# Optimization experiments

Measured on AMD Instinct MI355X. Metric: run time of the kernel, lower is better.

## Reference

```python
import jax, jax.numpy as jnp
import numpy as np

H, KV, HD, HID = 32, 8, 128, 4096
THETA, FACTOR, HI_FF, LO_FF, ORIG_MAX = 500000.0, 8.0, 4.0, 1.0, 8192


def _llama3_inv_freq():
    # standard Llama-3 rope scaling
    inv = 1.0 / (THETA ** (np.arange(0, HD, 2, dtype=np.float64) / HD))
    wavelen = 2.0 * np.pi / inv
    low_wl = ORIG_MAX / LO_FF
    high_wl = ORIG_MAX / HI_FF
    smooth = (ORIG_MAX / wavelen - LO_FF) / (HI_FF - LO_FF)
    scaled = np.where(wavelen > low_wl, inv / FACTOR, inv)
    mid = (wavelen <= low_wl) & (wavelen >= high_wl)
    scaled = np.where(mid, (1 - smooth) * inv / FACTOR + smooth * inv, scaled)
    return scaled.astype(np.float32)


def _rope_cos_sin(T):
    inv = _llama3_inv_freq()                       # [HD/2]
    pos = np.arange(T, dtype=np.float32)
    freqs = pos[:, None] * inv[None, :]            # [T, HD/2]
    emb = np.concatenate([freqs, freqs], axis=-1)  # [T, HD]
    return jnp.asarray(np.cos(emb)), jnp.asarray(np.sin(emb))


def _rotate_half(x):
    x1, x2 = jnp.split(x, 2, axis=-1)
    return jnp.concatenate([-x2, x1], axis=-1)


def setup_inputs() -> dict:
    key = jax.random.key(0)
    ks = jax.random.split(key, 5)
    s = 1.0 / np.sqrt(HID)
    return {
        "x": jax.random.normal(ks[0], (1, 2048, HID), jnp.float32),
        "wq": jax.random.normal(ks[1], (HID, H * HD), jnp.float32) * s,
        "wk": jax.random.normal(ks[2], (HID, KV * HD), jnp.float32) * s,
        "wv": jax.random.normal(ks[3], (HID, KV * HD), jnp.float32) * s,
        "wo": jax.random.normal(ks[4], (H * HD, HID), jnp.float32) * s,
    }


def reference(x, wq, wk, wv, wo):
    B, T, _ = x.shape
    q = (x @ wq).reshape(B, T, H, HD).transpose(0, 2, 1, 3)   # [B,H,T,D]
    k = (x @ wk).reshape(B, T, KV, HD).transpose(0, 2, 1, 3)  # [B,KV,T,D]
    v = (x @ wv).reshape(B, T, KV, HD).transpose(0, 2, 1, 3)
    cos, sin = _rope_cos_sin(T)                               # [T,D]
    q = q * cos + _rotate_half(q) * sin
    k = k * cos + _rotate_half(k) * sin
    rep = H // KV
    k = jnp.repeat(k, rep, axis=1)                            # [B,H,T,D]
    v = jnp.repeat(v, rep, axis=1)
    scores = jnp.einsum("bhtd,bhsd->bhts", q, k) * (1.0 / np.sqrt(HD))
    mask = jnp.tril(jnp.ones((T, T), dtype=bool))
    scores = jnp.where(mask, scores, -jnp.inf)
    att = jax.nn.softmax(scores, axis=-1)
    out = jnp.einsum("bhts,bhsd->bhtd", att, v)
    out = out.transpose(0, 2, 1, 3).reshape(B, T, H * HD)
    return out @ wo
```

## Files before the change

kernel.cpp:

```cpp
#include <hip/hip_runtime.h>
#include <math.h>

#define T_SEQ 2048
#define HID   4096
#define NH    32
#define NKV   8
#define HD    128
#define QCOLS (NH*HD)
#define KCOLS (NKV*HD)
#define KSTR  2048

typedef _Float16 f16;
typedef _Float16 f16x8 __attribute__((ext_vector_type(8)));
typedef _Float16 f16x4 __attribute__((ext_vector_type(4)));
typedef float f32x4 __attribute__((ext_vector_type(4)));

#define GLDS(g, l) __builtin_amdgcn_global_load_lds( \
    (const __attribute__((address_space(1))) void*)(g), \
    (__attribute__((address_space(3))) void*)(l), 16, 0, 0)

__global__ void rope_table(float* __restrict__ cosT, float* __restrict__ sinT) {
    int idx = blockIdx.x * blockDim.x + threadIdx.x;
    if (idx >= T_SEQ * 64) return;
    int t = idx >> 6, i = idx & 63;
    double inv = pow(500000.0, -(double)(2 * i) / 128.0);
    double wavelen = 6.283185307179586 / inv;
    const double lowwl = 8192.0, highwl = 2048.0;
    double scaled;
    if (wavelen > lowwl) {
        scaled = inv / 8.0;
    } else if (wavelen >= highwl) {
        double smooth = (8192.0 / wavelen - 1.0) / 3.0;
        scaled = (1.0 - smooth) * inv / 8.0 + smooth * inv;
    } else {
        scaled = inv;
    }
    float invf = (float)scaled;
    float phase = (float)t * invf;
    cosT[idx] = (float)cos((double)phase);
    sinT[idx] = (float)sin((double)phase);
}

__global__ void convert_f32_f16(const float* __restrict__ in, f16* __restrict__ out, int n8) {
    int i = blockIdx.x * blockDim.x + threadIdx.x;
    if (i >= n8) return;
    float4 a = *(const float4*)(in + (size_t)i * 8);
    float4 b = *(const float4*)(in + (size_t)i * 8 + 4);
    f16x8 v = {(f16)a.x, (f16)a.y, (f16)a.z, (f16)a.w, (f16)b.x, (f16)b.y, (f16)b.z, (f16)b.w};
    *(f16x8*)(out + (size_t)i * 8) = v;
}

__global__ __launch_bounds__(256) void transpose_f32_to_f16(const float* __restrict__ in,
                                                            f16* __restrict__ out,
                                                            int R, int ld) {
    __shared__ f16 t[64][72];
    const int tid = threadIdx.x;
    const int r0 = blockIdx.y * 64, c0 = blockIdx.x * 64;
#pragma unroll
    for (int i = 0; i < 4; ++i) {
        int r = i * 16 + (tid >> 4), c4 = (tid & 15) * 4;
        float4 v = *(const float4*)(in + (size_t)(r0 + r) * ld + c0 + c4);
        t[r][c4 + 0] = (f16)v.x; t[r][c4 + 1] = (f16)v.y;
        t[r][c4 + 2] = (f16)v.z; t[r][c4 + 3] = (f16)v.w;
    }
    __syncthreads();
    int n = tid >> 2, j0 = (tid & 3) * 16;
    f16x8 a, b;
#pragma unroll
    for (int j = 0; j < 8; ++j) { a[j] = t[j0 + j][n]; b[j] = t[j0 + 8 + j][n]; }
    *(f16x8*)(out + (size_t)(c0 + n) * R + r0 + j0) = a;
    *(f16x8*)(out + (size_t)(c0 + n) * R + r0 + j0 + 8) = b;
}

__global__ __launch_bounds__(256) void transpose_f16(const f16* __restrict__ in,
                                                     f16* __restrict__ out,
                                                     int R, int ld) {
    __shared__ f16 t[64][72];
    const int tid = threadIdx.x;
    const int r0 = blockIdx.y * 64, c0 = blockIdx.x * 64;
#pragma unroll
    for (int i = 0; i < 2; ++i) {
        int r = i * 32 + (tid >> 3), c8 = (tid & 7) * 8;
        f16x8 v = *(const f16x8*)(in + (size_t)(r0 + r) * ld + c0 + c8);
#pragma unroll
        for (int j = 0; j < 8; ++j) t[r][c8 + j] = v[j];
    }
    __syncthreads();
    int n = tid >> 2, j0 = (tid & 3) * 16;
    f16x8 a, b;
#pragma unroll
    for (int j = 0; j < 8; ++j) { a[j] = t[j0 + j][n]; b[j] = t[j0 + 8 + j][n]; }
    *(f16x8*)(out + (size_t)(c0 + n) * R + r0 + j0) = a;
    *(f16x8*)(out + (size_t)(c0 + n) * R + r0 + j0 + 8) = b;
}

template <typename OutT>
__global__ __launch_bounds__(256, 2) void gemm_f16(const f16* __restrict__ A,
                                                   const f16* __restrict__ Bt,
                                                   OutT* __restrict__ C,
                                                   int M, int ldc, int K) {
    __shared__ f16 As[2][128 * 64];
    __shared__ f16 Bs[2][128 * 64];
    const int tid = threadIdx.x;
    const int l = tid & 63;
    const int w = tid >> 6, wr = w >> 1, wc = w & 1;
    const int c16 = l & 15, g = l >> 4;
    const int m0 = blockIdx.y * 128, n0 = blockIdx.x * 128;

    f32x4 acc[4][4] = {};

    const int r_src = tid >> 3;
    const int colswz = ((tid & 7) * 8) ^ ((r_src & 7) << 3);
    const f16* gA = A + (size_t)(m0 + r_src) * K + colswz;
    const f16* gB = Bt + (size_t)(n0 + r_src) * K + colswz;

    auto stage = [&](f16* sA, f16* sB, int k0) {
#pragma unroll
        for (int i = 0; i < 4; ++i) {
            GLDS(gA + (size_t)(i * 32) * K + k0, sA + i * 2048 + tid * 8);
            GLDS(gB + (size_t)(i * 32) * K + k0, sB + i * 2048 + tid * 8);
        }
    };
    auto compute = [&](const f16* sA, const f16* sB) {
#pragma unroll
        for (int kk = 0; kk < 2; ++kk) {
            f16x8 af[4], bf[4];
#pragma unroll
            for (int mb = 0; mb < 4; ++mb) {
                int row = wr * 64 + mb * 16 + c16;
                af[mb] = *(const f16x8*)((const char*)sA + row * 128 +
                                         ((kk * 64 + g * 16) ^ ((row & 7) << 4)));
            }
#pragma unroll
            for (int nb = 0; nb < 4; ++nb) {
                int row = wc * 64 + nb * 16 + c16;
                bf[nb] = *(const f16x8*)((const char*)sB + row * 128 +
                                         ((kk * 64 + g * 16) ^ ((row & 7) << 4)));
            }
#pragma unroll
            for (int mb = 0; mb < 4; ++mb)
#pragma unroll
                for (int nb = 0; nb < 4; ++nb)
                    acc[mb][nb] = __builtin_amdgcn_mfma_f32_16x16x32_f16(af[mb], bf[nb], acc[mb][nb], 0, 0, 0);
        }
    };

    stage(As[0], Bs[0], 0);
    __syncthreads();
    int cur = 0;
    for (int k0 = 64; k0 < K; k0 += 64) {
        stage(As[cur ^ 1], Bs[cur ^ 1], k0);
        compute(As[cur], Bs[cur]);
        __syncthreads();
        cur ^= 1;
    }
    compute(As[cur], Bs[cur]);

#pragma unroll
    for (int mb = 0; mb < 4; ++mb)
#pragma unroll
        for (int nb = 0; nb < 4; ++nb)
#pragma unroll
            for (int r = 0; r < 4; ++r) {
                size_t row = m0 + wr * 64 + mb * 16 + g * 4 + r;
                C[row * ldc + n0 + wc * 64 + nb * 16 + c16] = (OutT)acc[mb][nb][r];
            }
}

__global__ void rope_apply_f16(f16* __restrict__ data, const float* __restrict__ cosT,
                               const float* __restrict__ sinT, int nheads, int stride) {
    int idx = blockIdx.x * blockDim.x + threadIdx.x;
    int lane = idx & 63;
    int row = idx >> 6;
    if (row >= T_SEQ * nheads) return;
    int t = row / nheads, h = row % nheads;
    f16* p = data + (size_t)t * stride + h * HD;
    float c = cosT[t * 64 + lane], s = sinT[t * 64 + lane];
    float x1 = (float)p[lane], x2 = (float)p[lane + 64];
    p[lane]      = (f16)(x1 * c - x2 * s);
    p[lane + 64] = (f16)(x2 * c + x1 * s);
}

__global__ __launch_bounds__(256, 2) void attn_f16(const f16* __restrict__ q,
                                                   const f16* __restrict__ k,
                                                   const f16* __restrict__ vt,
                                                   const float* __restrict__ cosT,
                                                   const float* __restrict__ sinT,
                                                   f16* __restrict__ outh) {
    __shared__ f16 Ks[2][64 * 128];
    __shared__ f16 Vs[2][128 * 64];
    __shared__ f16 Ps[4][16 * 72];
    const int tid = threadIdx.x;
    const int l = tid & 63, w = tid >> 6;
    const int c16 = l & 15, g = l >> 4;
    const int h = blockIdx.y, kvh = h >> 2;
    const float SCALE = 0.08838834764831845f;

    const int kr = tid >> 4, kboff = (tid & 15) * 16;
    const int vr = tid >> 3, vboff = (tid & 7) * 16;
    const char* kgb = (const char*)(k + kvh * HD);
    const char* vgb = (const char*)(vt + (size_t)(kvh * HD) * T_SEQ);

    auto stage = [&](int buf, int ch) {
#pragma unroll
        for (int i = 0; i < 4; ++i) {
            int r = i * 16 + kr;
            GLDS(kgb + (size_t)(ch * 64 + r) * (KSTR * 2) + (kboff ^ ((r & 7) << 4)),
                 (char*)Ks[buf] + i * 4096 + tid * 16);
            int d = i * 32 + vr;
            GLDS(vgb + (size_t)d * (T_SEQ * 2) + (size_t)(ch * 64) * 2 + (vboff ^ ((d & 7) << 4)),
                 (char*)Vs[buf] + i * 4096 + tid * 16);
        }
    };

    for (int pass = 0; pass < 2; ++pass) {
        const int qt = pass ? 31 - (int)blockIdx.x : (int)blockIdx.x;
        const int qrow = qt * 64 + w * 16 + c16;

        f16x8 qf[4];
        {
            const f16* qbase = q + (size_t)qrow * QCOLS + h * HD;
            f16x8 qraw[4];
#pragma unroll
            for (int ks = 0; ks < 4; ++ks) qraw[ks] = *(const f16x8*)(qbase + ks * 32 + g * 8);
            const float* cb = cosT + qrow * 64;
            const float* sb = sinT + qrow * 64;
#pragma unroll
            for (int ks = 0; ks < 2; ++ks) {
                int dbase = ks * 32 + g * 8;
                float4 c0 = *(const float4*)(cb + dbase);
                float4 c1 = *(const float4*)(cb + dbase + 4);
                float4 s0 = *(const float4*)(sb + dbase);
                float4 s1 = *(const float4*)(sb + dbase + 4);
                float cA[8] = {c0.x, c0.y, c0.z, c0.w, c1.x, c1.y, c1.z, c1.w};
                float sA[8] = {s0.x, s0.y, s0.z, s0.w, s1.x, s1.y, s1.z, s1.w};
#pragma unroll
                for (int j = 0; j < 8; ++j) {
                    float lo = (float)qraw[ks][j], hi = (float)qraw[ks + 2][j];
                    qf[ks][j]     = (f16)(lo * cA[j] - hi * sA[j]);
                    qf[ks + 2][j] = (f16)(hi * cA[j] + lo * sA[j]);
                }
            }
        }

        f32x4 o[8] = {};
        float mrun = -INFINITY, lrun = 0.f;

        stage(0, 0);
        __syncthreads();
        int cur = 0;
        for (int ch = 0; ch <= qt; ++ch) {
            if (ch < qt) stage(cur ^ 1, ch + 1);

            f32x4 st[4];
            __builtin_amdgcn_s_setprio(1);
#pragma unroll
            for (int kb = 0; kb < 4; ++kb) {
                f32x4 a = {};
#pragma unroll
                for (int ks = 0; ks < 4; ++ks) {
                    int row = kb * 16 + c16;
                    f16x8 kf = *(const f16x8*)((const char*)Ks[cur] + row * 256 +
                                               ((ks * 64 + g * 16) ^ ((row & 7) << 4)));
                    a = __builtin_amdgcn_mfma_f32_16x16x32_f16(kf, qf[ks], a, 0, 0, 0);
                }
                st[kb] = a;
            }
            __builtin_amdgcn_s_setprio(0);

            float p[16];
            float cmax = -INFINITY;
            const bool diag = (ch == qt);
#pragma unroll
            for (int kb = 0; kb < 4; ++kb)
#pragma unroll
                for (int r = 0; r < 4; ++r) {
                    float s = st[kb][r] * SCALE;
                    if (diag) {
                        int key = ch * 64 + kb * 16 + g * 4 + r;
                        if (key > qrow) s = -INFINITY;
                    }
                    p[kb * 4 + r] = s;
                    cmax = fmaxf(cmax, s);
                }
            cmax = fmaxf(cmax, __shfl_xor(cmax, 16));
            cmax = fmaxf(cmax, __shfl_xor(cmax, 32));

            float muse;
            if (__all(cmax <= mrun + 8.f)) {
                muse = mrun;
            } else {
                float mnew = fmaxf(mrun, cmax);
                float corr = __expf(mrun - mnew);
                lrun *= corr;
#pragma unroll
                for (int mb = 0; mb < 8; ++mb) o[mb] *= corr;
                mrun = mnew;
                muse = mnew;
            }
            float psum = 0.f;
#pragma unroll
            for (int i = 0; i < 16; ++i) { float e = __expf(p[i] - muse); p[i] = e; psum += e; }
            psum += __shfl_xor(psum, 16);
            psum += __shfl_xor(psum, 32);
            lrun += psum;

            f16* pw = Ps[w] + c16 * 72;
#pragma unroll
            for (int kb = 0; kb < 4; ++kb) {
                f16x4 q4 = {(f16)p[kb * 4], (f16)p[kb * 4 + 1], (f16)p[kb * 4 + 2], (f16)p[kb * 4 + 3]};
                *(f16x4*)(pw + kb * 16 + g * 4) = q4;
            }

            __builtin_amdgcn_s_setprio(1);
#pragma unroll
            for (int ks2 = 0; ks2 < 2; ++ks2) {
                f16x8 pf = *(const f16x8*)(Ps[w] + c16 * 72 + ks2 * 32 + g * 8);
#pragma unroll
                for (int mb = 0; mb < 8; ++mb) {
                    int row = mb * 16 + c16;
                    f16x8 vf = *(const f16x8*)((const char*)Vs[cur] + row * 128 +
                                               ((ks2 * 64 + g * 16) ^ ((row & 7) << 4)));
                    o[mb] = __builtin_amdgcn_mfma_f32_16x16x32_f16(vf, pf, o[mb], 0, 0, 0);
                }
            }
            __builtin_amdgcn_s_setprio(0);

            __syncthreads();
            cur ^= 1;
        }

        float invl = 1.f / lrun;
        f16* ob = outh + (size_t)qrow * QCOLS + h * HD;
#pragma unroll
        for (int mb = 0; mb < 8; ++mb) {
            f16x4 v = {(f16)(o[mb][0] * invl), (f16)(o[mb][1] * invl),
                       (f16)(o[mb][2] * invl), (f16)(o[mb][3] * invl)};
            *(f16x4*)(ob + mb * 16 + g * 4) = v;
        }
    }
}

extern "C" void kernel_launch(void* const* d_in, const int* in_sizes, int n_in,
                              void* d_out, int out_size, void* d_ws, size_t ws_size,
                              hipStream_t stream) {
    const float* x  = (const float*)d_in[0];
    const float* wq = (const float*)d_in[1];
    const float* wk = (const float*)d_in[2];
    const float* wv = (const float*)d_in[3];
    const float* wo = (const float*)d_in[4];
    float* out = (float*)d_out;

    char* ws = (char*)d_ws;
    const size_t MB = 1024ULL * 1024ULL;
    float* cosT = (float*)(ws);
    float* sinT = (float*)(ws + 512 * 1024ULL);
    f16* xh   = (f16*)(ws + 1 * MB);
    f16* atth = xh;
    f16* qh   = (f16*)(ws + 17 * MB);
    f16* kvh  = (f16*)(ws + 33 * MB);
    f16* wT   = (f16*)(ws + 41 * MB);
    f16* vtb  = (f16*)(ws + 73 * MB);

    rope_table<<<dim3((T_SEQ * 64 + 255) / 256), dim3(256), 0, stream>>>(cosT, sinT);
    convert_f32_f16<<<dim3(T_SEQ * HID / 8 / 256), dim3(256), 0, stream>>>(x, xh, T_SEQ * HID / 8);

    transpose_f32_to_f16<<<dim3(QCOLS / 64, HID / 64), dim3(256), 0, stream>>>(wq, wT, HID, QCOLS);
    gemm_f16<f16><<<dim3(QCOLS / 128, T_SEQ / 128), dim3(256), 0, stream>>>(
        xh, wT, qh, T_SEQ, QCOLS, HID);

    transpose_f32_to_f16<<<dim3(KCOLS / 64, HID / 64), dim3(256), 0, stream>>>(wk, wT, HID, KCOLS);
    transpose_f32_to_f16<<<dim3(KCOLS / 64, HID / 64), dim3(256), 0, stream>>>(
        wv, wT + (size_t)KCOLS * HID, HID, KCOLS);
    gemm_f16<f16><<<dim3(KSTR / 128, T_SEQ / 128), dim3(256), 0, stream>>>(
        xh, wT, kvh, T_SEQ, KSTR, HID);

    rope_apply_f16<<<dim3(T_SEQ * NKV * 64 / 256), dim3(256), 0, stream>>>(
        kvh, cosT, sinT, NKV, KSTR);

    transpose_f16<<<dim3(KCOLS / 64, T_SEQ / 64), dim3(256), 0, stream>>>(
        kvh + KCOLS, vtb, T_SEQ, KSTR);

    attn_f16<<<dim3(16, NH), dim3(256), 0, stream>>>(qh, kvh, vtb, cosT, sinT, atth);

    transpose_f32_to_f16<<<dim3(HID / 64, QCOLS / 64), dim3(256), 0, stream>>>(wo, wT, QCOLS, HID);
    gemm_f16<float><<<dim3(HID / 128, T_SEQ / 128), dim3(256), 0, stream>>>(
        atth, wT, out, T_SEQ, HID, QCOLS);
}
```

Before: 350.7 us.

## Process two query row groups per wave and drop K/V double buffering in attention

The attention kernel now runs 128 threads (2 waves) per block, and each wave handles two 16-row query groups, so every K and V fragment read from LDS feeds two MFMAs. LDS staging switches from a double-buffered prefetch to a single buffer loaded synchronously at the top of each chunk, with two barriers per iteration. The aim is to cut LDS read traffic per FLOP and the shared-memory footprint. The cost is higher register pressure from doubled accumulators, and global loads no longer overlap with compute, which may expose memory latency.

```diff
diff --git a/kernel.cpp b/kernel.cpp
--- a/kernel.cpp
+++ b/kernel.cpp
@@ -181,14 +181,14 @@
     p[lane + 64] = (f16)(x2 * c + x1 * s);
 }
 
-__global__ __launch_bounds__(256, 2) void attn_f16(const f16* __restrict__ q,
-                                                   const f16* __restrict__ k,
-                                                   const f16* __restrict__ vt,
-                                                   const float* __restrict__ cosT,
-                                                   const float* __restrict__ sinT,
-                                                   f16* __restrict__ outh) {
-    __shared__ f16 Ks[2][64 * 128];
-    __shared__ f16 Vs[2][128 * 64];
+__global__ __launch_bounds__(128) void attn_f16(const f16* __restrict__ q,
+                                                const f16* __restrict__ k,
+                                                const f16* __restrict__ vt,
+                                                const float* __restrict__ cosT,
+                                                const float* __restrict__ sinT,
+                                                f16* __restrict__ outh) {
+    __shared__ f16 Ks[64 * 128];
+    __shared__ f16 Vs[128 * 64];
     __shared__ f16 Ps[4][16 * 72];
     const int tid = threadIdx.x;
     const int l = tid & 63, w = tid >> 6;
@@ -201,24 +201,15 @@
     const char* kgb = (const char*)(k + kvh * HD);
     const char* vgb = (const char*)(vt + (size_t)(kvh * HD) * T_SEQ);
 
-    auto stage = [&](int buf, int ch) {
-#pragma unroll
-        for (int i = 0; i < 4; ++i) {
-            int r = i * 16 + kr;
-            GLDS(kgb + (size_t)(ch * 64 + r) * (KSTR * 2) + (kboff ^ ((r & 7) << 4)),
-                 (char*)Ks[buf] + i * 4096 + tid * 16);
-            int d = i * 32 + vr;
-            GLDS(vgb + (size_t)d * (T_SEQ * 2) + (size_t)(ch * 64) * 2 + (vboff ^ ((d & 7) << 4)),
-                 (char*)Vs[buf] + i * 4096 + tid * 16);
-        }
-    };
-
     for (int pass = 0; pass < 2; ++pass) {
         const int qt = pass ? 31 - (int)blockIdx.x : (int)blockIdx.x;
-        const int qrow = qt * 64 + w * 16 + c16;
-
-        f16x8 qf[4];
-        {
+        const int qrow0 = qt * 64 + w * 16 + c16;
+        const int qrow1 = qt * 64 + 32 + w * 16 + c16;
+
+        f16x8 qf[2][4];
+#pragma unroll
+        for (int gq = 0; gq < 2; ++gq) {
+            const int qrow = gq ? qrow1 : qrow0;
             const f16* qbase = q + (size_t)qrow * QCOLS + h * HD;
             f16x8 qraw[4];
 #pragma unroll
@@ -237,106 +228,123 @@
 #pragma unroll
                 for (int j = 0; j < 8; ++j) {
                     float lo = (float)qraw[ks][j], hi = (float)qraw[ks + 2][j];
-                    qf[ks][j]     = (f16)(lo * cA[j] - hi * sA[j]);
-                    qf[ks + 2][j] = (f16)(hi * cA[j] + lo * sA[j]);
-                }
-            }
-        }
-
-        f32x4 o[8] = {};
-        float mrun = -INFINITY, lrun = 0.f;
-
-        stage(0, 0);
-        __syncthreads();
-        int cur = 0;
+                    qf[gq][ks][j]     = (f16)(lo * cA[j] - hi * sA[j]);
+                    qf[gq][ks + 2][j] = (f16)(hi * cA[j] + lo * sA[j]);
+                }
+            }
+        }
+
+        f32x4 o[2][8] = {};
+        float mrun[2] = {-INFINITY, -INFINITY};
+        float lrun[2] = {0.f, 0.f};
+
         for (int ch = 0; ch <= qt; ++ch) {
-            if (ch < qt) stage(cur ^ 1, ch + 1);
-
-            f32x4 st[4];
+            __syncthreads();
+#pragma unroll
+            for (int i = 0; i < 8; ++i) {
+                int r = i * 8 + kr;
+                GLDS(kgb + (size_t)(ch * 64 + r) * (KSTR * 2) + (kboff ^ ((r & 7) << 4)),
+                     (char*)Ks + i * 2048 + tid * 16);
+                int d = i * 16 + vr;
+                GLDS(vgb + (size_t)d * (T_SEQ * 2) + (size_t)(ch * 64) * 2 + (vboff ^ ((d & 7) << 4)),
+                     (char*)Vs + i * 2048 + tid * 16);
+            }
+            __syncthreads();
+
+            f32x4 st[2][4];
             __builtin_amdgcn_s_setprio(1);
 #pragma unroll
             for (int kb = 0; kb < 4; ++kb) {
-                f32x4 a = {};
+                f32x4 a0 = {}, a1 = {};
 #pragma unroll
                 for (int ks = 0; ks < 4; ++ks) {
                     int row = kb * 16 + c16;
-                    f16x8 kf = *(const f16x8*)((const char*)Ks[cur] + row * 256 +
+                    f16x8 kf = *(const f16x8*)((const char*)Ks + row * 256 +
                                                ((ks * 64 + g * 16) ^ ((row & 7) << 4)));
-                    a = __builtin_amdgcn_mfma_f32_16x16x32_f16(kf, qf[ks], a, 0, 0, 0);
-                }
-                st[kb] = a;
+                    a0 = __builtin_amdgcn_mfma_f32_16x16x32_f16(kf, qf[0][ks], a0, 0, 0, 0);
+                    a1 = __builtin_amdgcn_mfma_f32_16x16x32_f16(kf, qf[1][ks], a1, 0, 0, 0);
+                }
+                st[0][kb] = a0; st[1][kb] = a1;
             }
             __builtin_amdgcn_s_setprio(0);
 
-            float p[16];
-            float cmax = -INFINITY;
             const bool diag = (ch == qt);
 #pragma unroll
-            for (int kb = 0; kb < 4; ++kb)
-#pragma unroll
-                for (int r = 0; r < 4; ++r) {
-                    float s = st[kb][r] * SCALE;
-                    if (diag) {
-                        int key = ch * 64 + kb * 16 + g * 4 + r;
-                        if (key > qrow) s = -INFINITY;
+            for (int gq = 0; gq < 2; ++gq) {
+                const int qrow = gq ? qrow1 : qrow0;
+                float p[16];
+                float cmax = -INFINITY;
+#pragma unroll
+                for (int kb = 0; kb < 4; ++kb)
+#pragma unroll
+                    for (int r = 0; r < 4; ++r) {
+                        float s = st[gq][kb][r] * SCALE;
+                        if (diag) {
+                            int key = ch * 64 + kb * 16 + g * 4 + r;
+                            if (key > qrow) s = -INFINITY;
+                        }
+                        p[kb * 4 + r] = s;
+                        cmax = fmaxf(cmax, s);
                     }
-                    p[kb * 4 + r] = s;
-                    cmax = fmaxf(cmax, s);
-                }
-            cmax = fmaxf(cmax, __shfl_xor(cmax, 16));
-            cmax = fmaxf(cmax, __shfl_xor(cmax, 32));
-
-            float muse;
-            if (__all(cmax <= mrun + 8.f)) {
-                muse = mrun;
-            } else {
-                float mnew = fmaxf(mrun, cmax);
-                float corr = __expf(mrun - mnew);
-                lrun *= corr;
-#pragma unroll
-                for (int mb = 0; mb < 8; ++mb) o[mb] *= corr;
-                mrun = mnew;
-                muse = mnew;
-            }
-            float psum = 0.f;
-#pragma unroll
-            for (int i = 0; i < 16; ++i) { float e = __expf(p[i] - muse); p[i] = e; psum += e; }
-            psum += __shfl_xor(psum, 16);
-            psum += __shfl_xor(psum, 32);
-            lrun += psum;
-
-            f16* pw = Ps[w] + c16 * 72;
-#pragma unroll
-            for (int kb = 0; kb < 4; ++kb) {
-                f16x4 q4 = {(f16)p[kb * 4], (f16)p[kb * 4 + 1], (f16)p[kb * 4 + 2], (f16)p[kb * 4 + 3]};
-                *(f16x4*)(pw + kb * 16 + g * 4) = q4;
+                cmax = fmaxf(cmax, __shfl_xor(cmax, 16));
+                cmax = fmaxf(cmax, __shfl_xor(cmax, 32));
+
+                float muse;
+                if (__all(cmax <= mrun[gq] + 8.f)) {
+                    muse = mrun[gq];
+                } else {
+                    float mnew = fmaxf(mrun[gq], cmax);
+                    float corr = __expf(mrun[gq] - mnew);
+                    lrun[gq] *= corr;
+#pragma unroll
+                    for (int mb = 0; mb < 8; ++mb) o[gq][mb] *= corr;
+                    mrun[gq] = mnew;
+                    muse = mnew;
+                }
+                float psum = 0.f;
+#pragma unroll
+                for (int i = 0; i < 16; ++i) { float e = __expf(p[i] - muse); p[i] = e; psum += e; }
+                psum += __shfl_xor(psum, 16);
+                psum += __shfl_xor(psum, 32);
+                lrun[gq] += psum;
+
+                f16* pw = Ps[w * 2 + gq] + c16 * 72;
+#pragma unroll
+                for (int kb = 0; kb < 4; ++kb) {
+                    f16x4 q4 = {(f16)p[kb * 4], (f16)p[kb * 4 + 1],
+                                (f16)p[kb * 4 + 2], (f16)p[kb * 4 + 3]};
+                    *(f16x4*)(pw + kb * 16 + g * 4) = q4;
+                }
             }
 
             __builtin_amdgcn_s_setprio(1);
 #pragma unroll
             for (int ks2 = 0; ks2 < 2; ++ks2) {
-                f16x8 pf = *(const f16x8*)(Ps[w] + c16 * 72 + ks2 * 32 + g * 8);
+                f16x8 pf0 = *(const f16x8*)(Ps[w * 2 + 0] + c16 * 72 + ks2 * 32 + g * 8);
+                f16x8 pf1 = *(const f16x8*)(Ps[w * 2 + 1] + c16 * 72 + ks2 * 32 + g * 8);
 #pragma unroll
                 for (int mb = 0; mb < 8; ++mb) {
                     int row = mb * 16 + c16;
-                    f16x8 vf = *(const f16x8*)((const char*)Vs[cur] + row * 128 +
+                    f16x8 vf = *(const f16x8*)((const char*)Vs + row * 128 +
                                                ((ks2 * 64 + g * 16) ^ ((row & 7) << 4)));
-                    o[mb] = __builtin_amdgcn_mfma_f32_16x16x32_f16(vf, pf, o[mb], 0, 0, 0);
+                    o[0][mb] = __builtin_amdgcn_mfma_f32_16x16x32_f16(vf, pf0, o[0][mb], 0, 0, 0);
+                    o[1][mb] = __builtin_amdgcn_mfma_f32_16x16x32_f16(vf, pf1, o[1][mb], 0, 0, 0);
                 }
             }
             __builtin_amdgcn_s_setprio(0);
-
-            __syncthreads();
-            cur ^= 1;
-        }
-
-        float invl = 1.f / lrun;
-        f16* ob = outh + (size_t)qrow * QCOLS + h * HD;
-#pragma unroll
-        for (int mb = 0; mb < 8; ++mb) {
-            f16x4 v = {(f16)(o[mb][0] * invl), (f16)(o[mb][1] * invl),
-                       (f16)(o[mb][2] * invl), (f16)(o[mb][3] * invl)};
-            *(f16x4*)(ob + mb * 16 + g * 4) = v;
+        }
+
+#pragma unroll
+        for (int gq = 0; gq < 2; ++gq) {
+            const int qrow = gq ? qrow1 : qrow0;
+            float invl = 1.f / lrun[gq];
+            f16* ob = outh + (size_t)qrow * QCOLS + h * HD;
+#pragma unroll
+            for (int mb = 0; mb < 8; ++mb) {
+                f16x4 v = {(f16)(o[gq][mb][0] * invl), (f16)(o[gq][mb][1] * invl),
+                           (f16)(o[gq][mb][2] * invl), (f16)(o[gq][mb][3] * invl)};
+                *(f16x4*)(ob + mb * 16 + g * 4) = v;
+            }
         }
     }
 }
@@ -381,7 +389,7 @@
     transpose_f16<<<dim3(KCOLS / 64, T_SEQ / 64), dim3(256), 0, stream>>>(
         kvh + KCOLS, vtb, T_SEQ, KSTR);
 
-    attn_f16<<<dim3(16, NH), dim3(256), 0, stream>>>(qh, kvh, vtb, cosT, sinT, atth);
+    attn_f16<<<dim3(16, NH), dim3(128), 0, stream>>>(qh, kvh, vtb, cosT, sinT, atth);
 
     transpose_f32_to_f16<<<dim3(HID / 64, QCOLS / 64), dim3(256), 0, stream>>>(wo, wT, QCOLS, HID);
     gemm_f16<float><<<dim3(HID / 128, T_SEQ / 128), dim3(256), 0, stream>>>(
```

Measured after the change: 367.5 us. 1.05x slower.

## Process paired causal query tiles together to share K/V chunk loads

Applied to the files above, without the earlier changes.

The attention kernel now keeps both paired query tiles (qt and 31-qt) live at once. For the first qtA+1 chunks, each staged K/V tile feeds MFMAs for both query tiles, so those chunks are loaded from global memory once instead of twice. The remaining chunks serve only the later tile. In exchange the K/V double buffering is dropped in favour of a single buffer with two barriers per chunk, which exposes load latency, and register pressure roughly doubles (two accumulator sets and two Q fragments). That pressure could cause spills or reduce occupancy under launch_bounds(256,2).

```diff
diff --git a/kernel.cpp b/kernel.cpp
--- a/kernel.cpp
+++ b/kernel.cpp
@@ -187,13 +187,14 @@
                                                    const float* __restrict__ cosT,
                                                    const float* __restrict__ sinT,
                                                    f16* __restrict__ outh) {
-    __shared__ f16 Ks[2][64 * 128];
-    __shared__ f16 Vs[2][128 * 64];
-    __shared__ f16 Ps[4][16 * 72];
+    __shared__ f16 Ks[64 * 128];
+    __shared__ f16 Vs[128 * 64];
+    __shared__ f16 Ps[8][16 * 72];
     const int tid = threadIdx.x;
     const int l = tid & 63, w = tid >> 6;
     const int c16 = l & 15, g = l >> 4;
     const int h = blockIdx.y, kvh = h >> 2;
+    const int qtA = blockIdx.x, qtB = 31 - (int)blockIdx.x;
     const float SCALE = 0.08838834764831845f;
 
     const int kr = tid >> 4, kboff = (tid & 15) * 16;
@@ -201,141 +202,194 @@
     const char* kgb = (const char*)(k + kvh * HD);
     const char* vgb = (const char*)(vt + (size_t)(kvh * HD) * T_SEQ);
 
-    auto stage = [&](int buf, int ch) {
+    auto stage = [&](int ch) {
 #pragma unroll
         for (int i = 0; i < 4; ++i) {
             int r = i * 16 + kr;
             GLDS(kgb + (size_t)(ch * 64 + r) * (KSTR * 2) + (kboff ^ ((r & 7) << 4)),
-                 (char*)Ks[buf] + i * 4096 + tid * 16);
+                 (char*)Ks + i * 4096 + tid * 16);
             int d = i * 32 + vr;
             GLDS(vgb + (size_t)d * (T_SEQ * 2) + (size_t)(ch * 64) * 2 + (vboff ^ ((d & 7) << 4)),
-                 (char*)Vs[buf] + i * 4096 + tid * 16);
+                 (char*)Vs + i * 4096 + tid * 16);
         }
     };
 
-    for (int pass = 0; pass < 2; ++pass) {
-        const int qt = pass ? 31 - (int)blockIdx.x : (int)blockIdx.x;
-        const int qrow = qt * 64 + w * 16 + c16;
-
-        f16x8 qf[4];
-        {
-            const f16* qbase = q + (size_t)qrow * QCOLS + h * HD;
-            f16x8 qraw[4];
-#pragma unroll
-            for (int ks = 0; ks < 4; ++ks) qraw[ks] = *(const f16x8*)(qbase + ks * 32 + g * 8);
-            const float* cb = cosT + qrow * 64;
-            const float* sb = sinT + qrow * 64;
-#pragma unroll
-            for (int ks = 0; ks < 2; ++ks) {
-                int dbase = ks * 32 + g * 8;
-                float4 c0 = *(const float4*)(cb + dbase);
-                float4 c1 = *(const float4*)(cb + dbase + 4);
-                float4 s0 = *(const float4*)(sb + dbase);
-                float4 s1 = *(const float4*)(sb + dbase + 4);
-                float cA[8] = {c0.x, c0.y, c0.z, c0.w, c1.x, c1.y, c1.z, c1.w};
-                float sA[8] = {s0.x, s0.y, s0.z, s0.w, s1.x, s1.y, s1.z, s1.w};
-#pragma unroll
-                for (int j = 0; j < 8; ++j) {
-                    float lo = (float)qraw[ks][j], hi = (float)qraw[ks + 2][j];
-                    qf[ks][j]     = (f16)(lo * cA[j] - hi * sA[j]);
-                    qf[ks + 2][j] = (f16)(hi * cA[j] + lo * sA[j]);
+    auto load_q = [&](int qrow, f16x8 (&qf)[4]) {
+        const f16* qbase = q + (size_t)qrow * QCOLS + h * HD;
+        f16x8 qraw[4];
+#pragma unroll
+        for (int ks = 0; ks < 4; ++ks) qraw[ks] = *(const f16x8*)(qbase + ks * 32 + g * 8);
+        const float* cb = cosT + qrow * 64;
+        const float* sb = sinT + qrow * 64;
+#pragma unroll
+        for (int ks = 0; ks < 2; ++ks) {
+            int dbase = ks * 32 + g * 8;
+            float4 c0 = *(const float4*)(cb + dbase);
+            float4 c1 = *(const float4*)(cb + dbase + 4);
+            float4 s0 = *(const float4*)(sb + dbase);
+            float4 s1 = *(const float4*)(sb + dbase + 4);
+            float cA[8] = {c0.x, c0.y, c0.z, c0.w, c1.x, c1.y, c1.z, c1.w};
+            float sA[8] = {s0.x, s0.y, s0.z, s0.w, s1.x, s1.y, s1.z, s1.w};
+#pragma unroll
+            for (int j = 0; j < 8; ++j) {
+                float lo = (float)qraw[ks][j], hi = (float)qraw[ks + 2][j];
+                qf[ks][j]     = (f16)(lo * cA[j] - hi * sA[j]);
+                qf[ks + 2][j] = (f16)(hi * cA[j] + lo * sA[j]);
+            }
+        }
+    };
+
+    auto smax = [&](f32x4 (&st)[4], f32x4 (&o)[8], float& mrun, float& lrun,
+                    int qrow, bool diag, int ch, f16* pw) {
+        float p[16];
+        float cmax = -INFINITY;
+#pragma unroll
+        for (int kb = 0; kb < 4; ++kb)
+#pragma unroll
+            for (int r = 0; r < 4; ++r) {
+                float s = st[kb][r] * SCALE;
+                if (diag) {
+                    int key = ch * 64 + kb * 16 + g * 4 + r;
+                    if (key > qrow) s = -INFINITY;
                 }
-            }
-        }
-
-        f32x4 o[8] = {};
-        float mrun = -INFINITY, lrun = 0.f;
-
-        stage(0, 0);
+                p[kb * 4 + r] = s;
+                cmax = fmaxf(cmax, s);
+            }
+        cmax = fmaxf(cmax, __shfl_xor(cmax, 16));
+        cmax = fmaxf(cmax, __shfl_xor(cmax, 32));
+        float muse;
+        if (__all(cmax <= mrun + 8.f)) {
+            muse = mrun;
+        } else {
+            float mnew = fmaxf(mrun, cmax);
+            float corr = __expf(mrun - mnew);
+            lrun *= corr;
+#pragma unroll
+            for (int mb = 0; mb < 8; ++mb) o[mb] *= corr;
+            mrun = mnew;
+            muse = mnew;
+        }
+        float psum = 0.f;
+#pragma unroll
+        for (int i = 0; i < 16; ++i) { float e = __expf(p[i] - muse); p[i] = e; psum += e; }
+        psum += __shfl_xor(psum, 16);
+        psum += __shfl_xor(psum, 32);
+        lrun += psum;
+#pragma unroll
+        for (int kb = 0; kb < 4; ++kb) {
+            f16x4 q4 = {(f16)p[kb * 4], (f16)p[kb * 4 + 1], (f16)p[kb * 4 + 2], (f16)p[kb * 4 + 3]};
+            *(f16x4*)(pw + kb * 16 + g * 4) = q4;
+        }
+    };
+
+    const int qrowA = qtA * 64 + w * 16 + c16;
+    const int qrowB = qtB * 64 + w * 16 + c16;
+    f16x8 qfA[4], qfB[4];
+    load_q(qrowA, qfA);
+    load_q(qrowB, qfB);
+
+    f32x4 oA[8] = {}, oB[8] = {};
+    float mA = -INFINITY, lA = 0.f, mB = -INFINITY, lB = 0.f;
+    f16* pwA = Ps[w * 2 + 0] + c16 * 72;
+    f16* pwB = Ps[w * 2 + 1] + c16 * 72;
+
+    for (int ch = 0; ch <= qtA; ++ch) {
         __syncthreads();
-        int cur = 0;
-        for (int ch = 0; ch <= qt; ++ch) {
-            if (ch < qt) stage(cur ^ 1, ch + 1);
-
-            f32x4 st[4];
-            __builtin_amdgcn_s_setprio(1);
-#pragma unroll
-            for (int kb = 0; kb < 4; ++kb) {
-                f32x4 a = {};
-#pragma unroll
-                for (int ks = 0; ks < 4; ++ks) {
-                    int row = kb * 16 + c16;
-                    f16x8 kf = *(const f16x8*)((const char*)Ks[cur] + row * 256 +
-                                               ((ks * 64 + g * 16) ^ ((row & 7) << 4)));
-                    a = __builtin_amdgcn_mfma_f32_16x16x32_f16(kf, qf[ks], a, 0, 0, 0);
-                }
-                st[kb] = a;
-            }
-            __builtin_amdgcn_s_setprio(0);
-
-            float p[16];
-            float cmax = -INFINITY;
-            const bool diag = (ch == qt);
-#pragma unroll
-            for (int kb = 0; kb < 4; ++kb)
-#pragma unroll
-                for (int r = 0; r < 4; ++r) {
-                    float s = st[kb][r] * SCALE;
-                    if (diag) {
-                        int key = ch * 64 + kb * 16 + g * 4 + r;
-                        if (key > qrow) s = -INFINITY;
-                    }
-                    p[kb * 4 + r] = s;
-                    cmax = fmaxf(cmax, s);
-                }
-            cmax = fmaxf(cmax, __shfl_xor(cmax, 16));
-            cmax = fmaxf(cmax, __shfl_xor(cmax, 32));
-
-            float muse;
-            if (__all(cmax <= mrun + 8.f)) {
-                muse = mrun;
-            } else {
-                float mnew = fmaxf(mrun, cmax);
-                float corr = __expf(mrun - mnew);
-                lrun *= corr;
-#pragma unroll
-                for (int mb = 0; mb < 8; ++mb) o[mb] *= corr;
-                mrun = mnew;
-                muse = mnew;
-            }
-            float psum = 0.f;
-#pragma unroll
-            for (int i = 0; i < 16; ++i) { float e = __expf(p[i] - muse); p[i] = e; psum += e; }
-            psum += __shfl_xor(psum, 16);
-            psum += __shfl_xor(psum, 32);
-            lrun += psum;
-
-            f16* pw = Ps[w] + c16 * 72;
-#pragma unroll
-            for (int kb = 0; kb < 4; ++kb) {
-                f16x4 q4 = {(f16)p[kb * 4], (f16)p[kb * 4 + 1], (f16)p[kb * 4 + 2], (f16)p[kb * 4 + 3]};
-                *(f16x4*)(pw + kb * 16 + g * 4) = q4;
-            }
-
-            __builtin_amdgcn_s_setprio(1);
-#pragma unroll
-            for (int ks2 = 0; ks2 < 2; ++ks2) {
-                f16x8 pf = *(const f16x8*)(Ps[w] + c16 * 72 + ks2 * 32 + g * 8);
-#pragma unroll
-                for (int mb = 0; mb < 8; ++mb) {
-                    int row = mb * 16 + c16;
-                    f16x8 vf = *(const f16x8*)((const char*)Vs[cur] + row * 128 +
-                                               ((ks2 * 64 + g * 16) ^ ((row & 7) << 4)));
-                    o[mb] = __builtin_amdgcn_mfma_f32_16x16x32_f16(vf, pf, o[mb], 0, 0, 0);
-                }
-            }
-            __builtin_amdgcn_s_setprio(0);
-
-            __syncthreads();
-            cur ^= 1;
-        }
-
-        float invl = 1.f / lrun;
-        f16* ob = outh + (size_t)qrow * QCOLS + h * HD;
+        stage(ch);
+        __syncthreads();
+
+        f32x4 stA[4], stB[4];
+        __builtin_amdgcn_s_setprio(1);
+#pragma unroll
+        for (int kb = 0; kb < 4; ++kb) {
+            f32x4 aA = {}, aB = {};
+#pragma unroll
+            for (int ks = 0; ks < 4; ++ks) {
+                int row = kb * 16 + c16;
+                f16x8 kf = *(const f16x8*)((const char*)Ks + row * 256 +
+                                           ((ks * 64 + g * 16) ^ ((row & 7) << 4)));
+                aB = __builtin_amdgcn_mfma_f32_16x16x32_f16(kf, qfB[ks], aB, 0, 0, 0);
+                aA = __builtin_amdgcn_mfma_f32_16x16x32_f16(kf, qfA[ks], aA, 0, 0, 0);
+            }
+            stB[kb] = aB; stA[kb] = aA;
+        }
+        __builtin_amdgcn_s_setprio(0);
+
+        smax(stB, oB, mB, lB, qrowB, false, ch, pwB);
+        smax(stA, oA, mA, lA, qrowA, ch == qtA, ch, pwA);
+
+        __builtin_amdgcn_s_setprio(1);
+#pragma unroll
+        for (int ks2 = 0; ks2 < 2; ++ks2) {
+            f16x8 pfB = *(const f16x8*)(pwB + ks2 * 32 + g * 8);
+            f16x8 pfA = *(const f16x8*)(pwA + ks2 * 32 + g * 8);
+#pragma unroll
+            for (int mb = 0; mb < 8; ++mb) {
+                int row = mb * 16 + c16;
+                f16x8 vf = *(const f16x8*)((const char*)Vs + row * 128 +
+                                           ((ks2 * 64 + g * 16) ^ ((row & 7) << 4)));
+                oB[mb] = __builtin_amdgcn_mfma_f32_16x16x32_f16(vf, pfB, oB[mb], 0, 0, 0);
+                oA[mb] = __builtin_amdgcn_mfma_f32_16x16x32_f16(vf, pfA, oA[mb], 0, 0, 0);
+            }
+        }
+        __builtin_amdgcn_s_setprio(0);
+    }
+
+    for (int ch = qtA + 1; ch <= qtB; ++ch) {
+        __syncthreads();
+        stage(ch);
+        __syncthreads();
+
+        f32x4 stB[4];
+        __builtin_amdgcn_s_setprio(1);
+#pragma unroll
+        for (int kb = 0; kb < 4; ++kb) {
+            f32x4 aB = {};
+#pragma unroll
+            for (int ks = 0; ks < 4; ++ks) {
+                int row = kb * 16 + c16;
+                f16x8 kf = *(const f16x8*)((const char*)Ks + row * 256 +
+                                           ((ks * 64 + g * 16) ^ ((row & 7) << 4)));
+                aB = __builtin_amdgcn_mfma_f32_16x16x32_f16(kf, qfB[ks], aB, 0, 0, 0);
+            }
+            stB[kb] = aB;
+        }
+        __builtin_amdgcn_s_setprio(0);
+
+        smax(stB, oB, mB, lB, qrowB, ch == qtB, ch, pwB);
+
+        __builtin_amdgcn_s_setprio(1);
+#pragma unroll
+        for (int ks2 = 0; ks2 < 2; ++ks2) {
+            f16x8 pfB = *(const f16x8*)(pwB + ks2 * 32 + g * 8);
+#pragma unroll
+            for (int mb = 0; mb < 8; ++mb) {
+                int row = mb * 16 + c16;
+                f16x8 vf = *(const f16x8*)((const char*)Vs + row * 128 +
+                                           ((ks2 * 64 + g * 16) ^ ((row & 7) << 4)));
+                oB[mb] = __builtin_amdgcn_mfma_f32_16x16x32_f16(vf, pfB, oB[mb], 0, 0, 0);
+            }
+        }
+        __builtin_amdgcn_s_setprio(0);
+    }
+
+    {
+        float invl = 1.f / lA;
+        f16* ob = outh + (size_t)qrowA * QCOLS + h * HD;
 #pragma unroll
         for (int mb = 0; mb < 8; ++mb) {
-            f16x4 v = {(f16)(o[mb][0] * invl), (f16)(o[mb][1] * invl),
-                       (f16)(o[mb][2] * invl), (f16)(o[mb][3] * invl)};
+            f16x4 v = {(f16)(oA[mb][0] * invl), (f16)(oA[mb][1] * invl),
+                       (f16)(oA[mb][2] * invl), (f16)(oA[mb][3] * invl)};
+            *(f16x4*)(ob + mb * 16 + g * 4) = v;
+        }
+    }
+    {
+        float invl = 1.f / lB;
+        f16* ob = outh + (size_t)qrowB * QCOLS + h * HD;
+#pragma unroll
+        for (int mb = 0; mb < 8; ++mb) {
+            f16x4 v = {(f16)(oB[mb][0] * invl), (f16)(oB[mb][1] * invl),
+                       (f16)(oB[mb][2] * invl), (f16)(oB[mb][3] * invl)};
             *(f16x4*)(ob + mb * 16 + g * 4) = v;
         }
     }
```

Measured after the change: 353.5 us. No clear change (+0.8%).

## Single-buffer attention K/V tiles for higher occupancy and reorder weight transposes

Applied to the files above, without the earlier changes.

The attention kernel drops double-buffered K/V shared memory in favor of a single buffer loaded synchronously each chunk, and raises the launch-bounds occupancy target from 2 to 3 blocks per CU. The aim is to hide latency through more resident waves instead of software prefetch, at the cost of losing load/compute overlap within a block. Separately, the Q weight transpose now goes into the output buffer as scratch so that all three projection transposes can run back to back before the GEMMs. This buffer reuse is safe only because the final GEMM overwrites the output later.

```diff
diff --git a/kernel.cpp b/kernel.cpp
--- a/kernel.cpp
+++ b/kernel.cpp
@@ -181,14 +181,14 @@
     p[lane + 64] = (f16)(x2 * c + x1 * s);
 }
 
-__global__ __launch_bounds__(256, 2) void attn_f16(const f16* __restrict__ q,
+__global__ __launch_bounds__(256, 3) void attn_f16(const f16* __restrict__ q,
                                                    const f16* __restrict__ k,
                                                    const f16* __restrict__ vt,
                                                    const float* __restrict__ cosT,
                                                    const float* __restrict__ sinT,
                                                    f16* __restrict__ outh) {
-    __shared__ f16 Ks[2][64 * 128];
-    __shared__ f16 Vs[2][128 * 64];
+    __shared__ f16 Ks[64 * 128];
+    __shared__ f16 Vs[128 * 64];
     __shared__ f16 Ps[4][16 * 72];
     const int tid = threadIdx.x;
     const int l = tid & 63, w = tid >> 6;
@@ -200,18 +200,6 @@
     const int vr = tid >> 3, vboff = (tid & 7) * 16;
     const char* kgb = (const char*)(k + kvh * HD);
     const char* vgb = (const char*)(vt + (size_t)(kvh * HD) * T_SEQ);
-
-    auto stage = [&](int buf, int ch) {
-#pragma unroll
-        for (int i = 0; i < 4; ++i) {
-            int r = i * 16 + kr;
-            GLDS(kgb + (size_t)(ch * 64 + r) * (KSTR * 2) + (kboff ^ ((r & 7) << 4)),
-                 (char*)Ks[buf] + i * 4096 + tid * 16);
-            int d = i * 32 + vr;
-            GLDS(vgb + (size_t)d * (T_SEQ * 2) + (size_t)(ch * 64) * 2 + (vboff ^ ((d & 7) << 4)),
-                 (char*)Vs[buf] + i * 4096 + tid * 16);
-        }
-    };
 
     for (int pass = 0; pass < 2; ++pass) {
         const int qt = pass ? 31 - (int)blockIdx.x : (int)blockIdx.x;
@@ -246,11 +234,18 @@
         f32x4 o[8] = {};
         float mrun = -INFINITY, lrun = 0.f;
 
-        stage(0, 0);
-        __syncthreads();
-        int cur = 0;
         for (int ch = 0; ch <= qt; ++ch) {
-            if (ch < qt) stage(cur ^ 1, ch + 1);
+            __syncthreads();
+#pragma unroll
+            for (int i = 0; i < 4; ++i) {
+                int r = i * 16 + kr;
+                GLDS(kgb + (size_t)(ch * 64 + r) * (KSTR * 2) + (kboff ^ ((r & 7) << 4)),
+                     (char*)Ks + i * 4096 + tid * 16);
+                int d = i * 32 + vr;
+                GLDS(vgb + (size_t)d * (T_SEQ * 2) + (size_t)(ch * 64) * 2 + (vboff ^ ((d & 7) << 4)),
+                     (char*)Vs + i * 4096 + tid * 16);
+            }
+            __syncthreads();
 
             f32x4 st[4];
             __builtin_amdgcn_s_setprio(1);
@@ -260,7 +255,7 @@
 #pragma unroll
                 for (int ks = 0; ks < 4; ++ks) {
                     int row = kb * 16 + c16;
-                    f16x8 kf = *(const f16x8*)((const char*)Ks[cur] + row * 256 +
+                    f16x8 kf = *(const f16x8*)((const char*)Ks + row * 256 +
                                                ((ks * 64 + g * 16) ^ ((row & 7) << 4)));
                     a = __builtin_amdgcn_mfma_f32_16x16x32_f16(kf, qf[ks], a, 0, 0, 0);
                 }
@@ -319,15 +314,12 @@
 #pragma unroll
                 for (int mb = 0; mb < 8; ++mb) {
                     int row = mb * 16 + c16;
-                    f16x8 vf = *(const f16x8*)((const char*)Vs[cur] + row * 128 +
+                    f16x8 vf = *(const f16x8*)((const char*)Vs + row * 128 +
                                                ((ks2 * 64 + g * 16) ^ ((row & 7) << 4)));
                     o[mb] = __builtin_amdgcn_mfma_f32_16x16x32_f16(vf, pf, o[mb], 0, 0, 0);
                 }
             }
             __builtin_amdgcn_s_setprio(0);
-
-            __syncthreads();
-            cur ^= 1;
         }
 
         float invl = 1.f / lrun;
@@ -359,21 +351,23 @@
     f16* atth = xh;
     f16* qh   = (f16*)(ws + 17 * MB);
     f16* kvh  = (f16*)(ws + 33 * MB);
-    f16* wT   = (f16*)(ws + 41 * MB);
+    f16* wkvT = (f16*)(ws + 41 * MB);
+    f16* woT  = (f16*)(ws + 41 * MB);
     f16* vtb  = (f16*)(ws + 73 * MB);
+    f16* wqT  = (f16*)d_out;
 
     rope_table<<<dim3((T_SEQ * 64 + 255) / 256), dim3(256), 0, stream>>>(cosT, sinT);
     convert_f32_f16<<<dim3(T_SEQ * HID / 8 / 256), dim3(256), 0, stream>>>(x, xh, T_SEQ * HID / 8);
 
-    transpose_f32_to_f16<<<dim3(QCOLS / 64, HID / 64), dim3(256), 0, stream>>>(wq, wT, HID, QCOLS);
+    transpose_f32_to_f16<<<dim3(QCOLS / 64, HID / 64), dim3(256), 0, stream>>>(wq, wqT, HID, QCOLS);
+    transpose_f32_to_f16<<<dim3(KCOLS / 64, HID / 64), dim3(256), 0, stream>>>(wk, wkvT, HID, KCOLS);
+    transpose_f32_to_f16<<<dim3(KCOLS / 64, HID / 64), dim3(256), 0, stream>>>(
+        wv, wkvT + (size_t)KCOLS * HID, HID, KCOLS);
+
     gemm_f16<f16><<<dim3(QCOLS / 128, T_SEQ / 128), dim3(256), 0, stream>>>(
-        xh, wT, qh, T_SEQ, QCOLS, HID);
-
-    transpose_f32_to_f16<<<dim3(KCOLS / 64, HID / 64), dim3(256), 0, stream>>>(wk, wT, HID, KCOLS);
-    transpose_f32_to_f16<<<dim3(KCOLS / 64, HID / 64), dim3(256), 0, stream>>>(
-        wv, wT + (size_t)KCOLS * HID, HID, KCOLS);
+        xh, wqT, qh, T_SEQ, QCOLS, HID);
     gemm_f16<f16><<<dim3(KSTR / 128, T_SEQ / 128), dim3(256), 0, stream>>>(
-        xh, wT, kvh, T_SEQ, KSTR, HID);
+        xh, wkvT, kvh, T_SEQ, KSTR, HID);
 
     rope_apply_f16<<<dim3(T_SEQ * NKV * 64 / 256), dim3(256), 0, stream>>>(
         kvh, cosT, sinT, NKV, KSTR);
@@ -383,7 +377,7 @@
 
     attn_f16<<<dim3(16, NH), dim3(256), 0, stream>>>(qh, kvh, vtb, cosT, sinT, atth);
 
-    transpose_f32_to_f16<<<dim3(HID / 64, QCOLS / 64), dim3(256), 0, stream>>>(wo, wT, QCOLS, HID);
+    transpose_f32_to_f16<<<dim3(HID / 64, QCOLS / 64), dim3(256), 0, stream>>>(wo, woT, QCOLS, HID);
     gemm_f16<float><<<dim3(HID / 128, T_SEQ / 128), dim3(256), 0, stream>>>(
-        atth, wT, out, T_SEQ, HID, QCOLS);
-}
+        atth, woT, out, T_SEQ, HID, QCOLS);
+}
```

After: 349.7 us. No clear change (-0.3%).
